# Performance work log

Hardware: AMD Instinct MI355X
Metric: run time of the kernel (lower is better)

The kernel has to match this reference:

```python
import jax, jax.numpy as jnp
import numpy as np

N = 40000   # query points
M = 40000   # support points
H = 32      # neighbors per query
CIN = 64
COUT = 64
KS = 3      # kernel points per dim
PDIM = 3
K = KS ** PDIM  # 27 kernel points
RADIUS = 1.0
KP_EXTENT = RADIUS / (KS - 1) * PDIM ** 0.5


def _kernel_points():
    # replicates KPConv.getKernelPoints: grid of KS^PDIM points in a ball of RADIUS
    xyz = np.linspace(-1.0, 1.0, KS)
    pts = np.meshgrid(*PDIM * [xyz])
    pts = np.vstack([p.flatten() for p in pts]).T  # [K, PDIM]
    pts = pts / PDIM ** 0.5
    return (pts * RADIUS).astype(np.float32)


def setup_inputs() -> dict:
    key = jax.random.key(0)
    k1, k2, k3, k4, k5 = jax.random.split(key, 5)
    q_pts = jax.random.uniform(k1, (N, PDIM), dtype=jnp.float32) * 10.0
    s_pts = jax.random.uniform(k2, (M, PDIM), dtype=jnp.float32) * 10.0
    neighb_inds = jax.random.randint(k3, (N, H), 0, M + 1)  # M == shadow index
    x = jax.random.normal(k4, (M, CIN), dtype=jnp.float32)
    # kaiming-uniform-like init for weights [K, CIN, COUT]
    bound = (6.0 / ((1.0 + 5.0) * CIN)) ** 0.5
    weights = jax.random.uniform(k5, (K, CIN, COUT), dtype=jnp.float32,
                                 minval=-bound, maxval=bound)
    kernel_points = jnp.asarray(_kernel_points())
    return {"q_pts": q_pts, "s_pts": s_pts, "neighb_inds": neighb_inds,
            "x": x, "weights": weights, "kernel_points": kernel_points}


def reference(q_pts, s_pts, neighb_inds, x, weights, kernel_points):
    # append shadow support point (far away) and zero shadow feature
    s_pts_p = jnp.concatenate(
        [s_pts, jnp.full((1, s_pts.shape[-1]), 1e6, dtype=s_pts.dtype)], axis=0)
    x_p = jnp.concatenate(
        [x, jnp.zeros((1, x.shape[-1]), dtype=x.dtype)], axis=0)

    neighbors = s_pts_p[neighb_inds] - q_pts[:, None, :]        # [N, H, 3]
    neighb_x = x_p[neighb_inds]                                  # [N, H, CIN]

    # distance of each neighbor to each kernel point
    diff = neighbors[:, :, None, :] - kernel_points              # [N, H, K, 3]
    sq_d = jnp.sum(diff * diff, axis=-1)                         # [N, H, K]
    all_w = jnp.clip(1.0 - jnp.sqrt(sq_d) / KP_EXTENT, 0.0)      # [N, H, K]

    # all_weights^T @ neighb_x  -> [N, K, CIN]
    weighted = jnp.einsum('nhk,nhc->nkc', all_w, neighb_x)
    # per-kernel-point matmul with weights [K, CIN, COUT], summed over K
    out = jnp.einsum('nkc,kco->no', weighted, weights)           # [N, COUT]
    return out
```

## Files before the change

### kernel.cpp

```cpp
#include <hip/hip_runtime.h>

typedef short bf16x8 __attribute__((ext_vector_type(8)));
typedef float f32x4  __attribute__((ext_vector_type(4)));

#define HN    32
#define CIN   64
#define KP    27
#define QB    64
#define CAPB  96
#define NTB   1024
#define OSTR  65

#define QB2   32
#define CAP2  64
#define OSTR2 68

#define INV_EXT 1.1547005383792517f
#define CUT2    3.4821f

__device__ __forceinline__ unsigned f2bf(float f){
    union{float fv;unsigned u;}v; v.fv=f;
    unsigned u=v.u;
    u += 0x7fffu + ((u>>16)&1u);
    return u>>16;
}

__global__ __launch_bounds__(256)
void kp_prep3(const float* __restrict__ s, const float* __restrict__ W,
              const float* __restrict__ xf,
              float4* __restrict__ o, unsigned short* __restrict__ Wt2,
              uint4* __restrict__ xb, int M)
{
    int tid = blockIdx.x*256 + threadIdx.x;
    if (tid < M) o[tid] = make_float4(s[tid*3+0], s[tid*3+1], s[tid*3+2], 0.f);
    if (tid < KP*8*64){
        int lane = tid & 63;
        int f  = (tid>>6) & 7;
        int kk = tid >> 9;
        int ot = f>>1, ks = f&1, gg = lane>>4;
        unsigned r[8];
#pragma unroll
        for (int j=0;j<8;++j)
            r[j] = f2bf(W[(size_t)kk*4096 + (size_t)(ks*32 + gg*8 + j)*64 + ot*16 + (lane&15)]);
        uint4 v; v.x=r[0]|(r[1]<<16); v.y=r[2]|(r[3]<<16); v.z=r[4]|(r[5]<<16); v.w=r[6]|(r[7]<<16);
        *(uint4*)&Wt2[(size_t)tid*8] = v;
    }
    if (tid < M*8){
        int row = tid>>3, c8 = tid&7;
        const float4* xr = (const float4*)(xf + (size_t)row*CIN);
        float4 f0=xr[c8*2], f1=xr[c8*2+1];
        uint4 v;
        v.x=f2bf(f0.x)|(f2bf(f0.y)<<16); v.y=f2bf(f0.z)|(f2bf(f0.w)<<16);
        v.z=f2bf(f1.x)|(f2bf(f1.y)<<16); v.w=f2bf(f1.z)|(f2bf(f1.w)<<16);
        xb[(size_t)row*8 + c8] = v;
    }
}

__device__ __forceinline__ bf16x8 ldBf(const unsigned short* __restrict__ Wt2, int k, int f, int lane){
    return *(const bf16x8*)(Wt2 + ((size_t)(k*8 + f)*64 + lane)*8);
}
__device__ __forceinline__ void loadB_w(const float* __restrict__ W, int k, int lane, int g,
                                        bf16x8 (&b)[8]){
#pragma unroll
    for (int f=0;f<8;++f){
        int ot=f>>1, ks=f&1;
        union{unsigned u[4]; bf16x8 v;} bb;
#pragma unroll
        for (int jj=0;jj<4;++jj){
            unsigned l0=f2bf(W[(size_t)k*4096 + (size_t)(ks*32+g*8+2*jj)*64   + ot*16+(lane&15)]);
            unsigned l1=f2bf(W[(size_t)k*4096 + (size_t)(ks*32+g*8+2*jj+1)*64 + ot*16+(lane&15)]);
            bb.u[jj]=l0|(l1<<16);
        }
        b[f]=bb.v;
    }
}

__global__ __launch_bounds__(256,4)
void kpconv_fused(const float* __restrict__ q_pts, const int* __restrict__ inds,
                  const uint4* __restrict__ xb, const float* __restrict__ kpts,
                  const float4* __restrict__ sp4, const unsigned short* __restrict__ Wt2,
                  float* __restrict__ out, int N, int M)
{
    __shared__ unsigned short rows[64*CIN];
    __shared__ __align__(16) float wlds[KP*64];
    __shared__ __align__(16) float outacc[QB2*OSTR2];
    __shared__ float qls[QB2*3];
    __shared__ float bx[CAP2], by[CAP2], bz[CAP2];
    __shared__ int bq[CAP2], bixs[CAP2];
    __shared__ int cnt;

    const int t    = threadIdx.x;
    const int lane = t & 63;
    const int wv   = t >> 6;
    const int g    = lane >> 4;
    const int r15  = lane & 15;
    const int nq0  = blockIdx.x * QB2;
    const int NP   = N*HN;

    for (int j=t; j<QB2*OSTR2; j+=256) outacc[j]=0.f;
    if (t < QB2*3){ int gi=nq0*3+t; qls[t]=(gi<N*3)? q_pts[gi]:0.f; }
    if (t < CAP2) bq[t]=0;
    if (t==0) cnt=0;
    __syncthreads();

    int idxv[4];
#pragma unroll
    for (int jj=0; jj<4; ++jj){
        int pair = nq0*HN + jj*256 + t;
        idxv[jj] = (pair < NP) ? inds[pair] : M;
    }
    float4 s4v[4];
#pragma unroll
    for (int jj=0; jj<4; ++jj){
        int ic = (idxv[jj] < M) ? idxv[jj] : 0;
        s4v[jj] = sp4[ic];
    }
#pragma unroll
    for (int jj=0; jj<4; ++jj){
        if (idxv[jj] < M){
            int q = (jj*256 + t) >> 5;
            float px=s4v[jj].x-qls[q*3], py=s4v[jj].y-qls[q*3+1], pz=s4v[jj].z-qls[q*3+2];
            if (px*px+py*py+pz*pz <= CUT2){
                int sl = atomicAdd(&cnt, 1);
                if (sl < CAP2){ bx[sl]=px; by[sl]=py; bz[sl]=pz; bq[sl]=q; bixs[sl]=idxv[jj]; }
            }
        }
    }
    __syncthreads();
    const int total = cnt;

    auto process = [&](int cc){
        const int nrow = (cc + 15) & ~15;
        int itA=t, itB=t+256;
        int rlA=itA>>3, c8A=itA&7, rlB=itB>>3, c8B=itB&7;
        bool vA=(rlA<cc), vB=(rlB<cc);
        bool wrA=(rlA<nrow), wrB=(rlB<nrow);
        int ixA = vA ? bixs[rlA] : bixs[0];
        int ixB = vB ? bixs[rlB] : bixs[0];
        uint4 dA = xb[(size_t)ixA*8 + c8A];
        uint4 dB = xb[(size_t)ixB*8 + c8B];
        for (int i=t; i<KP*64; i+=256){
            int row = i&63;
            if (row >= nrow) continue;
            int k = i>>6;
            float w=0.f;
            if (row < cc){
                float dx=bx[row]-kpts[k*3+0];
                float dy=by[row]-kpts[k*3+1];
                float dz=bz[row]-kpts[k*3+2];
                w = fmaxf(1.f - sqrtf(dx*dx+dy*dy+dz*dz)*INV_EXT, 0.f);
            }
            wlds[i]=w;
        }
        if (wrA){
            uint4 v; v.x=0u; v.y=0u; v.z=0u; v.w=0u;
            if (vA) v = dA;
            *(uint4*)((char*)rows + rlA*128 + ((c8A*16)^((rlA&7)<<4))) = v;
        }
        if (wrB){
            uint4 v; v.x=0u; v.y=0u; v.z=0u; v.w=0u;
            if (vB) v = dB;
            *(uint4*)((char*)rows + rlB*128 + ((c8B*16)^((rlB&7)<<4))) = v;
        }
        __syncthreads();

        const char* rb = (const char*)rows;
        bool rtv[4];
        bf16x8 A0[4], A1[4];
#pragma unroll
        for (int rt=0; rt<4; ++rt){
            rtv[rt] = (rt*16) < cc;
            int row = rt*16 + r15;
            int rc  = rtv[rt] ? row : r15;
            A0[rt] = *(const bf16x8*)(rb + rc*128 + (( g*16)   ^((rc&7)<<4)));
            A1[rt] = *(const bf16x8*)(rb + rc*128 + ((64+g*16) ^((rc&7)<<4)));
        }
        f32x4 acc[4];
#pragma unroll
        for (int rt=0; rt<4; ++rt){ f32x4 z={0.f,0.f,0.f,0.f}; acc[rt]=z; }

        const int f0 = wv*2, f1 = wv*2+1;
        bf16x8 Bc0 = ldBf(Wt2, 0, f0, lane);
        bf16x8 Bc1 = ldBf(Wt2, 0, f1, lane);
#pragma unroll 1
        for (int k=0; k<KP; ++k){
            int kn = (k+1 < KP) ? (k+1) : k;
            bf16x8 Bn0 = ldBf(Wt2, kn, f0, lane);
            bf16x8 Bn1 = ldBf(Wt2, kn, f1, lane);
            const float* wk = &wlds[k*64];
#pragma unroll
            for (int rt=0; rt<4; ++rt){
                if (!rtv[rt]) continue;
                f32x4 w4 = *(const f32x4*)(wk + rt*16 + g*4);
                bool act = __any(w4[0]>0.f || w4[1]>0.f || w4[2]>0.f || w4[3]>0.f);
                if (act){
                    f32x4 c={0.f,0.f,0.f,0.f};
                    c = __builtin_amdgcn_mfma_f32_16x16x32_bf16(A0[rt], Bc0, c, 0,0,0);
                    c = __builtin_amdgcn_mfma_f32_16x16x32_bf16(A1[rt], Bc1, c, 0,0,0);
                    acc[rt][0] += w4[0]*c[0];
                    acc[rt][1] += w4[1]*c[1];
                    acc[rt][2] += w4[2]*c[2];
                    acc[rt][3] += w4[3]*c[3];
                }
            }
            Bc0 = Bn0; Bc1 = Bn1;
        }
#pragma unroll
        for (int rt=0; rt<4; ++rt){
            if (!rtv[rt]) continue;
            int rbase = rt*16 + g*4;
#pragma unroll
            for (int rr=0; rr<4; ++rr){
                float val = acc[rt][rr];
                int qv = bq[rbase+rr];
                if (val != 0.f)
                    atomicAdd(&outacc[qv*OSTR2 + wv*16 + r15], val);
            }
        }
        __syncthreads();
    };

    if (total <= CAP2){
        if (total > 0) process(total);
    } else {
        for (int w=0; w<(QB2*HN)/64; ++w){
            __syncthreads();
            if (t==0) cnt=0;
            __syncthreads();
            if (t < 64){
                int pl = w*64 + t, pair = nq0*HN + pl;
                if (pair < NP){
                    int idx = inds[pair];
                    if ((unsigned)idx < (unsigned)M){
                        int q = pl >> 5;
                        float4 s4 = sp4[idx];
                        float px=s4.x-qls[q*3], py=s4.y-qls[q*3+1], pz=s4.z-qls[q*3+2];
                        if (px*px+py*py+pz*pz <= CUT2){
                            int sl = atomicAdd(&cnt, 1);
                            bx[sl]=px; by[sl]=py; bz[sl]=pz; bq[sl]=q; bixs[sl]=idx;
                        }
                    }
                }
            }
            __syncthreads();
            if (cnt > 0) process(cnt);
        }
    }
    __syncthreads();

    for (int j=t; j<QB2*16; j+=256){
        int q=j>>4, o4=j&15, n=nq0+q;
        if (n < N)
            ((float4*)out)[(size_t)n*16 + o4] = *(const float4*)&outacc[q*OSTR2 + o4*4];
    }
}


__global__ __launch_bounds__(NTB)
void kpconv6(const float* __restrict__ q_pts, const float* __restrict__ s_pts,
             const int* __restrict__ inds, const float* __restrict__ x,
             const float* __restrict__ W, const float* __restrict__ kpts,
             float* __restrict__ out, int N, int M)
{
    __shared__ float qls[QB*3];
    __shared__ float posx[CAPB], posy[CAPB], posz[CAPB];
    __shared__ int   eqb[CAPB], eidxb[CAPB];
    __shared__ unsigned short rows[CAPB*CIN];
    __shared__ float outacc[QB*OSTR];
    __shared__ int   cnt;

    const int t    = threadIdx.x;
    const int lane = t & 63;
    const int wv   = t >> 6;
    const int g    = lane >> 4;
    const int r15  = lane & 15;
    const int nq0  = blockIdx.x * QB;

    const int k0 = wv, k1 = wv + 16;
    const bool has2 = (k1 < KP);

    bf16x8 B0[8], B1[8];
    loadB_w(W, k0, lane, g, B0);
    loadB_w(W, has2 ? k1 : k0, lane, g, B1);
    const float k0x=kpts[k0*3+0], k0y=kpts[k0*3+1], k0z=kpts[k0*3+2];
    float k1x=0.f,k1y=0.f,k1z=0.f;
    if (has2){ k1x=kpts[k1*3+0]; k1y=kpts[k1*3+1]; k1z=kpts[k1*3+2]; }

    for (int j=t; j<QB*OSTR; j+=NTB) outacc[j]=0.f;
    for (int j=t; j<QB*3;   j+=NTB){ int gi=nq0*3+j; qls[j]=(gi<N*3)? q_pts[gi]:0.f; }
    if (t==0) cnt=0;
    __syncthreads();

    auto process = [&](int cc){
        if (cc<=0) return;
        const int ntile=(cc+15)>>4, nrow=ntile*16;
        for (int j=cc+t; j<nrow; j+=NTB){ posx[j]=1e9f; posy[j]=1e9f; posz[j]=1e9f; eqb[j]=0; }
        for (int it=t; it<nrow*8; it+=NTB){
            int e=it>>3, c8=it&7;
            uint4 v; v.x=0u; v.y=0u; v.z=0u; v.w=0u;
            if (e<cc){
                const float4* xr=(const float4*)(x+(size_t)eidxb[e]*CIN);
                float4 f0=xr[c8*2], f1=xr[c8*2+1];
                v.x=f2bf(f0.x)|(f2bf(f0.y)<<16); v.y=f2bf(f0.z)|(f2bf(f0.w)<<16);
                v.z=f2bf(f1.x)|(f2bf(f1.y)<<16); v.w=f2bf(f1.z)|(f2bf(f1.w)<<16);
            }
            int ba=e*128+((c8*16)^((e&7)<<4));
            *(uint4*)((char*)rows+ba)=v;
        }
        __syncthreads();
        for (int tile=0; tile<ntile; ++tile){
            const char* rb=(const char*)rows;
            int row=tile*16+r15;
            bf16x8 a0=*(const bf16x8*)(rb+row*128+((g*16)    ^((row&7)<<4)));
            bf16x8 a1=*(const bf16x8*)(rb+row*128+((64+g*16) ^((row&7)<<4)));
            int rbase=tile*16+g*4;
            float w0[4], w1[4]; int qq[4];
#pragma unroll
            for (int r=0;r<4;++r){
                float sx=posx[rbase+r], sy=posy[rbase+r], sz=posz[rbase+r];
                qq[r]=eqb[rbase+r];
                float dx=sx-k0x, dy=sy-k0y, dz=sz-k0z;
                w0[r]=fmaxf(1.f-sqrtf(dx*dx+dy*dy+dz*dz)*INV_EXT,0.f);
                float ex=sx-k1x, ey=sy-k1y, ez=sz-k1z;
                float w1r=fmaxf(1.f-sqrtf(ex*ex+ey*ey+ez*ez)*INV_EXT,0.f);
                w1[r]=has2? w1r : 0.f;
            }
#pragma unroll
            for (int ot=0;ot<4;++ot){
                f32x4 c={0.f,0.f,0.f,0.f};
                c=__builtin_amdgcn_mfma_f32_16x16x32_bf16(a0,B0[2*ot],c,0,0,0);
                c=__builtin_amdgcn_mfma_f32_16x16x32_bf16(a1,B0[2*ot+1],c,0,0,0);
                f32x4 d={0.f,0.f,0.f,0.f};
                if (has2){
                    d=__builtin_amdgcn_mfma_f32_16x16x32_bf16(a0,B1[2*ot],d,0,0,0);
                    d=__builtin_amdgcn_mfma_f32_16x16x32_bf16(a1,B1[2*ot+1],d,0,0,0);
                }
#pragma unroll
                for (int r=0;r<4;++r){
                    float val=w0[r]*c[r]+w1[r]*d[r];
                    if (val!=0.f) atomicAdd(&outacc[qq[r]*OSTR+ot*16+r15], val);
                }
            }
        }
        __syncthreads();
    };

    for (int it=t; it<QB*HN; it+=NTB){
        int q=it>>5, h=it&31, n=nq0+q;
        bool inr=false; int idx=0; float px=0.f,py=0.f,pz=0.f;
        if (n<N){
            idx=inds[(size_t)n*HN+h];
            if ((unsigned)idx<(unsigned)M){
                float sx=s_pts[idx*3], sy=s_pts[idx*3+1], sz=s_pts[idx*3+2];
                px=sx-qls[q*3]; py=sy-qls[q*3+1]; pz=sz-qls[q*3+2];
                inr=(px*px+py*py+pz*pz)<=CUT2;
            }
        }
        if (inr){
            int sl=atomicAdd(&cnt,1);
            if (sl<CAPB){ eqb[sl]=q; eidxb[sl]=idx; posx[sl]=px; posy[sl]=py; posz[sl]=pz; }
        }
    }
    __syncthreads();
    const int total=cnt;

    if (total<=CAPB){
        process(total);
    } else {
        for (int w=0; w<(QB*HN)/64; ++w){
            __syncthreads();
            if (t==0) cnt=0;
            __syncthreads();
            if (t<64){
                int pair=w*64+t;
                int q=pair>>5, h=pair&31, n=nq0+q;
                if (n<N){
                    int idx=inds[(size_t)n*HN+h];
                    if ((unsigned)idx<(unsigned)M){
                        float sx=s_pts[idx*3], sy=s_pts[idx*3+1], sz=s_pts[idx*3+2];
                        float px=sx-qls[q*3], py=sy-qls[q*3+1], pz=sz-qls[q*3+2];
                        if (px*px+py*py+pz*pz<=CUT2){
                            int sl=atomicAdd(&cnt,1);
                            eqb[sl]=q; eidxb[sl]=idx; posx[sl]=px; posy[sl]=py; posz[sl]=pz;
                        }
                    }
                }
            }
            __syncthreads();
            process(cnt);
        }
    }
    __syncthreads();

    for (int j=t; j<QB*CIN; j+=NTB){
        int q=j>>6, o=j&63, n=nq0+q;
        if (n<N) out[(size_t)n*CIN+o]=outacc[q*OSTR+o];
    }
}

extern "C" void kernel_launch(void* const* d_in, const int* in_sizes, int n_in,
                              void* d_out, int out_size, void* d_ws, size_t ws_size,
                              hipStream_t stream)
{
    const float* q_pts=(const float*)d_in[0];
    const float* s_pts=(const float*)d_in[1];
    const int*   inds =(const int*)d_in[2];
    const float* x    =(const float*)d_in[3];
    const float* W    =(const float*)d_in[4];
    const float* kpts =(const float*)d_in[5];
    float* outp=(float*)d_out;
    int N=in_sizes[0]/3;
    int M=in_sizes[1]/3;

    char* wsb=(char*)d_ws;
    float4* sp4=(float4*)wsb;
    const size_t WT2B = (size_t)KP*8*64*8*2;
    unsigned short* Wt2=(unsigned short*)(wsb + (size_t)M*16);
    uint4* xb = (uint4*)(wsb + (size_t)M*16 + WT2B);

    size_t need = (size_t)M*16 + WT2B + (size_t)M*128;

    if (ws_size >= need){
        int prepUnits = M*8;
        if (prepUnits < M) prepUnits = M;
        if (prepUnits < KP*8*64) prepUnits = KP*8*64;
        hipLaunchKernelGGL(kp_prep3, dim3((prepUnits+255)/256), dim3(256), 0, stream,
                           s_pts, W, x, sp4, Wt2, xb, M);
        int nblocks = (N + QB2 - 1) / QB2;
        hipLaunchKernelGGL(kpconv_fused, dim3(nblocks), dim3(256), 0, stream,
                           q_pts, inds, xb, kpts, sp4, Wt2, outp, N, M);
        return;
    }

    hipLaunchKernelGGL(kpconv6, dim3((N+QB-1)/QB), dim3(NTB), 0, stream,
                       q_pts, s_pts, inds, x, W, kpts, outp, N, M);
}
```

Baseline: 46.69 us.

## Gather and convert neighbor features to bf16 inside fused kernel, drop prep pass

Removes the pre-pass that converted all of x to a bf16 copy in workspace. Instead, each thread that accepts a neighbor within the cutoff reads that neighbor's fp32 feature row directly, converts it to bf16, and writes it into the swizzled LDS tile. It also hoists the A-fragment and first B loads before the weight computation and drops the trailing barrier in the tile routine. This avoids writing and re-reading a full bf16 copy of x (only a small fraction of neighbors pass the cutoff), at the cost of a serialized per-thread 256-byte gather that is less coalesced and an extra zeroing of the LDS tile.

```diff
diff --git a/kernel.cpp b/kernel.cpp
--- a/kernel.cpp
+++ b/kernel.cpp
@@ -26,10 +26,8 @@
 }
 
 __global__ __launch_bounds__(256)
-void kp_prep3(const float* __restrict__ s, const float* __restrict__ W,
-              const float* __restrict__ xf,
-              float4* __restrict__ o, unsigned short* __restrict__ Wt2,
-              uint4* __restrict__ xb, int M)
+void kp_prep2(const float* __restrict__ s, const float* __restrict__ W,
+              float4* __restrict__ o, unsigned short* __restrict__ Wt2, int M)
 {
     int tid = blockIdx.x*256 + threadIdx.x;
     if (tid < M) o[tid] = make_float4(s[tid*3+0], s[tid*3+1], s[tid*3+2], 0.f);
@@ -45,15 +43,6 @@
         uint4 v; v.x=r[0]|(r[1]<<16); v.y=r[2]|(r[3]<<16); v.z=r[4]|(r[5]<<16); v.w=r[6]|(r[7]<<16);
         *(uint4*)&Wt2[(size_t)tid*8] = v;
     }
-    if (tid < M*8){
-        int row = tid>>3, c8 = tid&7;
-        const float4* xr = (const float4*)(xf + (size_t)row*CIN);
-        float4 f0=xr[c8*2], f1=xr[c8*2+1];
-        uint4 v;
-        v.x=f2bf(f0.x)|(f2bf(f0.y)<<16); v.y=f2bf(f0.z)|(f2bf(f0.w)<<16);
-        v.z=f2bf(f1.x)|(f2bf(f1.y)<<16); v.w=f2bf(f1.z)|(f2bf(f1.w)<<16);
-        xb[(size_t)row*8 + c8] = v;
-    }
 }
 
 __device__ __forceinline__ bf16x8 ldBf(const unsigned short* __restrict__ Wt2, int k, int f, int lane){
@@ -77,7 +66,7 @@
 
 __global__ __launch_bounds__(256,4)
 void kpconv_fused(const float* __restrict__ q_pts, const int* __restrict__ inds,
-                  const uint4* __restrict__ xb, const float* __restrict__ kpts,
+                  const float* __restrict__ x, const float* __restrict__ kpts,
                   const float4* __restrict__ sp4, const unsigned short* __restrict__ Wt2,
                   float* __restrict__ out, int N, int M)
 {
@@ -86,7 +75,7 @@
     __shared__ __align__(16) float outacc[QB2*OSTR2];
     __shared__ float qls[QB2*3];
     __shared__ float bx[CAP2], by[CAP2], bz[CAP2];
-    __shared__ int bq[CAP2], bixs[CAP2];
+    __shared__ int bq[CAP2];
     __shared__ int cnt;
 
     const int t    = threadIdx.x;
@@ -98,6 +87,8 @@
     const int NP   = N*HN;
 
     for (int j=t; j<QB2*OSTR2; j+=256) outacc[j]=0.f;
+    { uint4 z; z.x=0u; z.y=0u; z.z=0u; z.w=0u;
+      ((uint4*)rows)[t] = z; ((uint4*)rows)[t+256] = z; }
     if (t < QB2*3){ int gi=nq0*3+t; qls[t]=(gi<N*3)? q_pts[gi]:0.f; }
     if (t < CAP2) bq[t]=0;
     if (t==0) cnt=0;
@@ -122,23 +113,42 @@
             float px=s4v[jj].x-qls[q*3], py=s4v[jj].y-qls[q*3+1], pz=s4v[jj].z-qls[q*3+2];
             if (px*px+py*py+pz*pz <= CUT2){
                 int sl = atomicAdd(&cnt, 1);
-                if (sl < CAP2){ bx[sl]=px; by[sl]=py; bz[sl]=pz; bq[sl]=q; bixs[sl]=idxv[jj]; }
+                if (sl < CAP2){
+                    bq[sl]=q; bx[sl]=px; by[sl]=py; bz[sl]=pz;
+                    const float4* xr = (const float4*)(x + (size_t)idxv[jj]*CIN);
+                    char* rbase = (char*)rows + sl*128;
+                    const int sw = (sl&7)<<4;
+#pragma unroll
+                    for (int c8=0;c8<8;++c8){
+                        float4 f0=xr[2*c8], f1=xr[2*c8+1];
+                        uint4 v;
+                        v.x=f2bf(f0.x)|(f2bf(f0.y)<<16); v.y=f2bf(f0.z)|(f2bf(f0.w)<<16);
+                        v.z=f2bf(f1.x)|(f2bf(f1.y)<<16); v.w=f2bf(f1.z)|(f2bf(f1.w)<<16);
+                        *(uint4*)(rbase + ((c8*16)^sw)) = v;
+                    }
+                }
             }
         }
     }
     __syncthreads();
     const int total = cnt;
 
-    auto process = [&](int cc){
+    auto processTile = [&](int cc){
         const int nrow = (cc + 15) & ~15;
-        int itA=t, itB=t+256;
-        int rlA=itA>>3, c8A=itA&7, rlB=itB>>3, c8B=itB&7;
-        bool vA=(rlA<cc), vB=(rlB<cc);
-        bool wrA=(rlA<nrow), wrB=(rlB<nrow);
-        int ixA = vA ? bixs[rlA] : bixs[0];
-        int ixB = vB ? bixs[rlB] : bixs[0];
-        uint4 dA = xb[(size_t)ixA*8 + c8A];
-        uint4 dB = xb[(size_t)ixB*8 + c8B];
+        const char* rb = (const char*)rows;
+        bool rtv[4];
+        bf16x8 A0[4], A1[4];
+#pragma unroll
+        for (int rt=0; rt<4; ++rt){
+            rtv[rt] = (rt*16) < cc;
+            int row = rt*16 + r15;
+            int rc  = rtv[rt] ? row : r15;
+            A0[rt] = *(const bf16x8*)(rb + rc*128 + (( g*16)   ^((rc&7)<<4)));
+            A1[rt] = *(const bf16x8*)(rb + rc*128 + ((64+g*16) ^((rc&7)<<4)));
+        }
+        const int f0 = wv*2, f1 = wv*2+1;
+        bf16x8 Bc0 = ldBf(Wt2, 0, f0, lane);
+        bf16x8 Bc1 = ldBf(Wt2, 0, f1, lane);
         for (int i=t; i<KP*64; i+=256){
             int row = i&63;
             if (row >= nrow) continue;
@@ -152,36 +162,12 @@
             }
             wlds[i]=w;
         }
-        if (wrA){
-            uint4 v; v.x=0u; v.y=0u; v.z=0u; v.w=0u;
-            if (vA) v = dA;
-            *(uint4*)((char*)rows + rlA*128 + ((c8A*16)^((rlA&7)<<4))) = v;
-        }
-        if (wrB){
-            uint4 v; v.x=0u; v.y=0u; v.z=0u; v.w=0u;
-            if (vB) v = dB;
-            *(uint4*)((char*)rows + rlB*128 + ((c8B*16)^((rlB&7)<<4))) = v;
-        }
         __syncthreads();
 
-        const char* rb = (const char*)rows;
-        bool rtv[4];
-        bf16x8 A0[4], A1[4];
-#pragma unroll
-        for (int rt=0; rt<4; ++rt){
-            rtv[rt] = (rt*16) < cc;
-            int row = rt*16 + r15;
-            int rc  = rtv[rt] ? row : r15;
-            A0[rt] = *(const bf16x8*)(rb + rc*128 + (( g*16)   ^((rc&7)<<4)));
-            A1[rt] = *(const bf16x8*)(rb + rc*128 + ((64+g*16) ^((rc&7)<<4)));
-        }
         f32x4 acc[4];
 #pragma unroll
         for (int rt=0; rt<4; ++rt){ f32x4 z={0.f,0.f,0.f,0.f}; acc[rt]=z; }
 
-        const int f0 = wv*2, f1 = wv*2+1;
-        bf16x8 Bc0 = ldBf(Wt2, 0, f0, lane);
-        bf16x8 Bc1 = ldBf(Wt2, 0, f1, lane);
 #pragma unroll 1
         for (int k=0; k<KP; ++k){
             int kn = (k+1 < KP) ? (k+1) : k;
@@ -217,14 +203,15 @@
                     atomicAdd(&outacc[qv*OSTR2 + wv*16 + r15], val);
             }
         }
-        __syncthreads();
     };
 
     if (total <= CAP2){
-        if (total > 0) process(total);
+        if (total > 0) processTile(total);
     } else {
         for (int w=0; w<(QB2*HN)/64; ++w){
             __syncthreads();
+            { uint4 z; z.x=0u; z.y=0u; z.z=0u; z.w=0u;
+              ((uint4*)rows)[t] = z; ((uint4*)rows)[t+256] = z; }
             if (t==0) cnt=0;
             __syncthreads();
             if (t < 64){
@@ -237,13 +224,24 @@
                         float px=s4.x-qls[q*3], py=s4.y-qls[q*3+1], pz=s4.z-qls[q*3+2];
                         if (px*px+py*py+pz*pz <= CUT2){
                             int sl = atomicAdd(&cnt, 1);
-                            bx[sl]=px; by[sl]=py; bz[sl]=pz; bq[sl]=q; bixs[sl]=idx;
+                            bq[sl]=q; bx[sl]=px; by[sl]=py; bz[sl]=pz;
+                            const float4* xr = (const float4*)(x + (size_t)idx*CIN);
+                            char* rbase = (char*)rows + sl*128;
+                            const int sw = (sl&7)<<4;
+#pragma unroll
+                            for (int c8=0;c8<8;++c8){
+                                float4 f0=xr[2*c8], f1=xr[2*c8+1];
+                                uint4 v;
+                                v.x=f2bf(f0.x)|(f2bf(f0.y)<<16); v.y=f2bf(f0.z)|(f2bf(f0.w)<<16);
+                                v.z=f2bf(f1.x)|(f2bf(f1.y)<<16); v.w=f2bf(f1.z)|(f2bf(f1.w)<<16);
+                                *(uint4*)(rbase + ((c8*16)^sw)) = v;
+                            }
                         }
                     }
                 }
             }
             __syncthreads();
-            if (cnt > 0) process(cnt);
+            if (cnt > 0) processTile(cnt);
         }
     }
     __syncthreads();
@@ -416,19 +414,16 @@
     float4* sp4=(float4*)wsb;
     const size_t WT2B = (size_t)KP*8*64*8*2;
     unsigned short* Wt2=(unsigned short*)(wsb + (size_t)M*16);
-    uint4* xb = (uint4*)(wsb + (size_t)M*16 + WT2B);
-
-    size_t need = (size_t)M*16 + WT2B + (size_t)M*128;
+
+    size_t need = (size_t)M*16 + WT2B;
 
     if (ws_size >= need){
-        int prepUnits = M*8;
-        if (prepUnits < M) prepUnits = M;
-        if (prepUnits < KP*8*64) prepUnits = KP*8*64;
-        hipLaunchKernelGGL(kp_prep3, dim3((prepUnits+255)/256), dim3(256), 0, stream,
-                           s_pts, W, x, sp4, Wt2, xb, M);
+        int prepN = (M > KP*8*64) ? M : KP*8*64;
+        hipLaunchKernelGGL(kp_prep2, dim3((prepN+255)/256), dim3(256), 0, stream,
+                           s_pts, W, sp4, Wt2, M);
         int nblocks = (N + QB2 - 1) / QB2;
         hipLaunchKernelGGL(kpconv_fused, dim3(nblocks), dim3(256), 0, stream,
-                           q_pts, inds, xb, kpts, sp4, Wt2, outp, N, M);
+                           q_pts, inds, x, kpts, sp4, Wt2, outp, N, M);
         return;
     }
 
```

Measured after the change: 50.85 us. 1.09x slower.
